# Performance work log

Hardware: AMD Instinct MI355X
Metric: run time of the kernel (lower is better)

The kernel has to match this reference:

```python
import jax, jax.numpy as jnp
import numpy as np

C = 16          # n_comp per axis
G = 300         # grid resolution per axis
N = 2_000_000   # number of sampled points


def setup_inputs() -> dict:
    key = jax.random.key(0)
    k1, k2, k3 = jax.random.split(key, 3)
    # normalized coordinates in [-1, 1] (grid_sample convention)
    xyz = jax.random.uniform(k1, (N, 3), minval=-1.0, maxval=1.0, dtype=jnp.float32)
    planes = 0.1 * jax.random.normal(k2, (3, C, G, G), dtype=jnp.float32)  # (axis, C, H, W)
    lines = 0.1 * jax.random.normal(k3, (3, C, G), dtype=jnp.float32)      # (axis, C, G)
    return {"xyz": xyz, "planes": planes, "lines": lines}


def _lerp_idx(coord, size):
    # align_corners=True mapping: [-1,1] -> [0, size-1]
    x = (coord + 1.0) * 0.5 * (size - 1)
    x0 = jnp.clip(jnp.floor(x), 0, size - 1).astype(jnp.int32)
    x1 = jnp.minimum(x0 + 1, size - 1)
    w = x - x0.astype(x.dtype)
    return x0, x1, w


def _sample_plane(plane, gx, gy):
    # plane: (C, H, W); gx, gy: (N,) in [-1,1]; grid x indexes W, y indexes H
    H, W = plane.shape[-2:]
    x0, x1, wx = _lerp_idx(gx, W)
    y0, y1, wy = _lerp_idx(gy, H)
    v00 = plane[:, y0, x0]  # (C, N)
    v01 = plane[:, y0, x1]
    v10 = plane[:, y1, x0]
    v11 = plane[:, y1, x1]
    return (v00 * (1 - wx) + v01 * wx) * (1 - wy) + (v10 * (1 - wx) + v11 * wx) * wy


def _sample_line(line, g):
    # line: (C, G); g: (N,) in [-1,1]; width dim of original (G,1) grid is size 1 -> ignored
    Gs = line.shape[-1]
    y0, y1, wy = _lerp_idx(g, Gs)
    return line[:, y0] * (1 - wy) + line[:, y1] * wy  # (C, N)


def reference(xyz, planes, lines):
    # matMode[i] = axes != i; plane i sampled at (x=xyz[id_0], y=xyz[id_1])
    matMode = ((1, 2), (0, 2), (0, 1))
    feats = []
    for i in range(3):
        a, b = matMode[i]
        p = _sample_plane(planes[i], xyz[:, a], xyz[:, b])  # (C, N)
        l = _sample_line(lines[i], xyz[:, i])               # (C, N)
        feats.append(p * l)
    return jnp.concatenate(feats, axis=0)  # (3*C, N)
```

## Files before the change

### kernel.cpp

```cpp
#include <hip/hip_runtime.h>

#define CC 16
#define GG 300

typedef unsigned int  u32;
typedef unsigned short u16;

__device__ __forceinline__ float bf_lo(u32 u) { union { u32 i; float f; } v; v.i = u << 16;          return v.f; }
__device__ __forceinline__ float bf_hi(u32 u) { union { u32 i; float f; } v; v.i = u & 0xffff0000u;  return v.f; }
__device__ __forceinline__ u16 f2bf(float f) {
    union { float f; u32 i; } v; v.f = f;
    u32 r = v.i + 0x7fffu + ((v.i >> 16) & 1u);
    return (u16)(r >> 16);
}

__global__ void transpose_planes_k(const float* __restrict__ src, u32* __restrict__ dst) {
    int tid = blockIdx.x * blockDim.x + threadIdx.x;
    const int total = 3 * GG * GG;
    if (tid >= total) return;
    int x = tid % GG;
    int y = (tid / GG) % GG;
    int i = tid / (GG * GG);
    u32 packed[8];
#pragma unroll
    for (int h = 0; h < 8; ++h) {
        float a = src[((size_t)(i * CC + 2 * h)     * GG + y) * GG + x];
        float b = src[((size_t)(i * CC + 2 * h + 1) * GG + y) * GG + x];
        packed[h] = (u32)f2bf(a) | ((u32)f2bf(b) << 16);
    }
    uint4* d = (uint4*)(dst + (size_t)tid * 8);
    d[0] = make_uint4(packed[0], packed[1], packed[2], packed[3]);
    d[1] = make_uint4(packed[4], packed[5], packed[6], packed[7]);
}

__global__ void transpose_lines_k(const float* __restrict__ src, u32* __restrict__ dst) {
    int tid = blockIdx.x * blockDim.x + threadIdx.x;
    const int total = 3 * GG;
    if (tid >= total) return;
    int g = tid % GG;
    int i = tid / GG;
    u32 packed[8];
#pragma unroll
    for (int h = 0; h < 8; ++h) {
        float a = src[(size_t)(i * CC + 2 * h)     * GG + g];
        float b = src[(size_t)(i * CC + 2 * h + 1) * GG + g];
        packed[h] = (u32)f2bf(a) | ((u32)f2bf(b) << 16);
    }
    uint4* d = (uint4*)(dst + (size_t)tid * 8);
    d[0] = make_uint4(packed[0], packed[1], packed[2], packed[3]);
    d[1] = make_uint4(packed[4], packed[5], packed[6], packed[7]);
}

__device__ __forceinline__ float bilerp(float v00, float v01, float v10, float v11,
                                        float wx, float wy) {
    float ox = 1.0f - wx, oy = 1.0f - wy;
    return (v00 * ox + v01 * wx) * oy + (v10 * ox + v11 * wx) * wy;
}

__global__ __launch_bounds__(256) void sample_k(
    const float* __restrict__ xyz,
    const u32* __restrict__ planesT,
    const u32* __restrict__ linesT,
    float* __restrict__ out, int N)
{
    int n = blockIdx.x * blockDim.x + threadIdx.x;
    if (n >= N) return;

    float crd[3];
    crd[0] = xyz[3 * n + 0];
    crd[1] = xyz[3 * n + 1];
    crd[2] = xyz[3 * n + 2];

    int i0[3], i1[3];
    float w[3];
#pragma unroll
    for (int k = 0; k < 3; ++k) {
        float xk = (crd[k] + 1.0f) * 0.5f * (float)(GG - 1);
        float xf = floorf(xk);
        xf = fminf(fmaxf(xf, 0.0f), (float)(GG - 1));
        i0[k] = (int)xf;
        i1[k] = min(i0[k] + 1, GG - 1);
        w[k] = xk - xf;
    }

    const int mata[3] = {1, 0, 0};
    const int matb[3] = {2, 2, 1};

#pragma unroll
    for (int i = 0; i < 3; ++i) {
        const int xa0 = i0[mata[i]], xa1 = i1[mata[i]];
        const int yb0 = i0[matb[i]], yb1 = i1[matb[i]];
        const float wx = w[mata[i]], wy = w[matb[i]], wz = w[i];
        const float oz = 1.0f - wz;

        const u32* pb = planesT + (size_t)i * (GG * GG * 8);
        const uint4* c00 = (const uint4*)(pb + (size_t)(yb0 * GG + xa0) * 8);
        const uint4* c01 = (const uint4*)(pb + (size_t)(yb0 * GG + xa1) * 8);
        const uint4* c10 = (const uint4*)(pb + (size_t)(yb1 * GG + xa0) * 8);
        const uint4* c11 = (const uint4*)(pb + (size_t)(yb1 * GG + xa1) * 8);
        const uint4* lp0 = (const uint4*)(linesT + ((size_t)i * GG + i0[i]) * 8);
        const uint4* lp1 = (const uint4*)(linesT + ((size_t)i * GG + i1[i]) * 8);

        uint4 A00 = c00[0], B00 = c00[1];
        uint4 A01 = c01[0], B01 = c01[1];
        uint4 A10 = c10[0], B10 = c10[1];
        uint4 A11 = c11[0], B11 = c11[1];
        uint4 AL0 = lp0[0], BL0 = lp0[1];
        uint4 AL1 = lp1[0], BL1 = lp1[1];

        u32 r00[8] = {A00.x, A00.y, A00.z, A00.w, B00.x, B00.y, B00.z, B00.w};
        u32 r01[8] = {A01.x, A01.y, A01.z, A01.w, B01.x, B01.y, B01.z, B01.w};
        u32 r10[8] = {A10.x, A10.y, A10.z, A10.w, B10.x, B10.y, B10.z, B10.w};
        u32 r11[8] = {A11.x, A11.y, A11.z, A11.w, B11.x, B11.y, B11.z, B11.w};
        u32 rl0[8] = {AL0.x, AL0.y, AL0.z, AL0.w, BL0.x, BL0.y, BL0.z, BL0.w};
        u32 rl1[8] = {AL1.x, AL1.y, AL1.z, AL1.w, BL1.x, BL1.y, BL1.z, BL1.w};

#pragma unroll
        for (int u = 0; u < 8; ++u) {
            float p0 = bilerp(bf_lo(r00[u]), bf_lo(r01[u]), bf_lo(r10[u]), bf_lo(r11[u]), wx, wy);
            float p1 = bilerp(bf_hi(r00[u]), bf_hi(r01[u]), bf_hi(r10[u]), bf_hi(r11[u]), wx, wy);
            float l0 = bf_lo(rl0[u]) * oz + bf_lo(rl1[u]) * wz;
            float l1 = bf_hi(rl0[u]) * oz + bf_hi(rl1[u]) * wz;
            size_t row = (size_t)(i * CC + 2 * u);
            __builtin_nontemporal_store(p0 * l0, &out[row * (size_t)N + n]);
            __builtin_nontemporal_store(p1 * l1, &out[(row + 1) * (size_t)N + n]);
        }
    }
}

__global__ __launch_bounds__(256) void sample_fallback_k(
    const float* __restrict__ xyz,
    const float* __restrict__ planes,
    const float* __restrict__ lines,
    float* __restrict__ out, int N)
{
    int n = blockIdx.x * blockDim.x + threadIdx.x;
    if (n >= N) return;

    float crd[3];
    crd[0] = xyz[3 * n + 0];
    crd[1] = xyz[3 * n + 1];
    crd[2] = xyz[3 * n + 2];

    int i0[3], i1[3];
    float w[3];
#pragma unroll
    for (int k = 0; k < 3; ++k) {
        float xk = (crd[k] + 1.0f) * 0.5f * (float)(GG - 1);
        float xf = floorf(xk);
        xf = fminf(fmaxf(xf, 0.0f), (float)(GG - 1));
        i0[k] = (int)xf;
        i1[k] = min(i0[k] + 1, GG - 1);
        w[k] = xk - xf;
    }

    const int mata[3] = {1, 0, 0};
    const int matb[3] = {2, 2, 1};

    for (int i = 0; i < 3; ++i) {
        const int xa0 = i0[mata[i]], xa1 = i1[mata[i]];
        const int yb0 = i0[matb[i]], yb1 = i1[matb[i]];
        const float wx = w[mata[i]], wy = w[matb[i]], wz = w[i];
        const float oz = 1.0f - wz;
        const float* pb = planes + (size_t)i * (CC * GG * GG);
        const float* lb = lines + (size_t)i * (CC * GG);
        for (int c = 0; c < CC; ++c) {
            const float* pc = pb + (size_t)c * (GG * GG);
            float p = bilerp(pc[yb0 * GG + xa0], pc[yb0 * GG + xa1],
                             pc[yb1 * GG + xa0], pc[yb1 * GG + xa1], wx, wy);
            float l = lb[c * GG + i0[i]] * oz + lb[c * GG + i1[i]] * wz;
            out[(size_t)(i * CC + c) * (size_t)N + n] = p * l;
        }
    }
}

extern "C" void kernel_launch(void* const* d_in, const int* in_sizes, int n_in,
                              void* d_out, int out_size, void* d_ws, size_t ws_size,
                              hipStream_t stream) {
    const float* xyz    = (const float*)d_in[0];
    const float* planes = (const float*)d_in[1];
    const float* lines  = (const float*)d_in[2];
    float* out = (float*)d_out;
    const int N = in_sizes[0] / 3;

    const size_t planesT_u32 = (size_t)3 * GG * GG * 8;
    const size_t linesT_u32  = (size_t)3 * GG * 8;
    const size_t need = (planesT_u32 + linesT_u32) * sizeof(u32);

    if (ws_size >= need) {
        u32* planesT = (u32*)d_ws;
        u32* linesT  = planesT + planesT_u32;
        {
            int total = 3 * GG * GG;
            transpose_planes_k<<<(total + 255) / 256, 256, 0, stream>>>(planes, planesT);
        }
        {
            int total = 3 * GG;
            transpose_lines_k<<<(total + 255) / 256, 256, 0, stream>>>(lines, linesT);
        }
        sample_k<<<(N + 255) / 256, 256, 0, stream>>>(xyz, planesT, linesT, out, N);
    } else {
        sample_fallback_k<<<(N + 255) / 256, 256, 0, stream>>>(xyz, planes, lines, out, N);
    }
}
```

Measured before the change: 623.0 us.

## Split sampling kernel across planes so each block handles one plane

The grid is now three times larger and each block processes a single plane for its 256 points, instead of one thread looping over all three planes. The aim is more parallelism and shorter per-thread dependency chains, with each block's gathers confined to one plane's transposed table so the cache works on a smaller footprint. The cost is that xyz is read and index/weight math is done three times per point. The xyz loads also become nontemporal, which may work against reuse of those coordinates across the three plane blocks.

```diff
diff --git a/kernel.cpp b/kernel.cpp
--- a/kernel.cpp
+++ b/kernel.cpp
@@ -57,19 +57,20 @@
     return (v00 * ox + v01 * wx) * oy + (v10 * ox + v11 * wx) * wy;
 }
 
-__global__ __launch_bounds__(256) void sample_k(
+__global__ __launch_bounds__(256) void sample_plane_k(
     const float* __restrict__ xyz,
     const u32* __restrict__ planesT,
     const u32* __restrict__ linesT,
-    float* __restrict__ out, int N)
+    float* __restrict__ out, int N, int nbPer)
 {
-    int n = blockIdx.x * blockDim.x + threadIdx.x;
+    const int plane = blockIdx.x / nbPer;
+    const int n = (blockIdx.x % nbPer) * 256 + threadIdx.x;
     if (n >= N) return;
 
     float crd[3];
-    crd[0] = xyz[3 * n + 0];
-    crd[1] = xyz[3 * n + 1];
-    crd[2] = xyz[3 * n + 2];
+    crd[0] = __builtin_nontemporal_load(xyz + 3 * (size_t)n + 0);
+    crd[1] = __builtin_nontemporal_load(xyz + 3 * (size_t)n + 1);
+    crd[2] = __builtin_nontemporal_load(xyz + 3 * (size_t)n + 2);
 
     int i0[3], i1[3];
     float w[3];
@@ -85,46 +86,45 @@
 
     const int mata[3] = {1, 0, 0};
     const int matb[3] = {2, 2, 1};
-
-#pragma unroll
-    for (int i = 0; i < 3; ++i) {
-        const int xa0 = i0[mata[i]], xa1 = i1[mata[i]];
-        const int yb0 = i0[matb[i]], yb1 = i1[matb[i]];
-        const float wx = w[mata[i]], wy = w[matb[i]], wz = w[i];
-        const float oz = 1.0f - wz;
-
-        const u32* pb = planesT + (size_t)i * (GG * GG * 8);
-        const uint4* c00 = (const uint4*)(pb + (size_t)(yb0 * GG + xa0) * 8);
-        const uint4* c01 = (const uint4*)(pb + (size_t)(yb0 * GG + xa1) * 8);
-        const uint4* c10 = (const uint4*)(pb + (size_t)(yb1 * GG + xa0) * 8);
-        const uint4* c11 = (const uint4*)(pb + (size_t)(yb1 * GG + xa1) * 8);
-        const uint4* lp0 = (const uint4*)(linesT + ((size_t)i * GG + i0[i]) * 8);
-        const uint4* lp1 = (const uint4*)(linesT + ((size_t)i * GG + i1[i]) * 8);
-
-        uint4 A00 = c00[0], B00 = c00[1];
-        uint4 A01 = c01[0], B01 = c01[1];
-        uint4 A10 = c10[0], B10 = c10[1];
-        uint4 A11 = c11[0], B11 = c11[1];
-        uint4 AL0 = lp0[0], BL0 = lp0[1];
-        uint4 AL1 = lp1[0], BL1 = lp1[1];
-
-        u32 r00[8] = {A00.x, A00.y, A00.z, A00.w, B00.x, B00.y, B00.z, B00.w};
-        u32 r01[8] = {A01.x, A01.y, A01.z, A01.w, B01.x, B01.y, B01.z, B01.w};
-        u32 r10[8] = {A10.x, A10.y, A10.z, A10.w, B10.x, B10.y, B10.z, B10.w};
-        u32 r11[8] = {A11.x, A11.y, A11.z, A11.w, B11.x, B11.y, B11.z, B11.w};
-        u32 rl0[8] = {AL0.x, AL0.y, AL0.z, AL0.w, BL0.x, BL0.y, BL0.z, BL0.w};
-        u32 rl1[8] = {AL1.x, AL1.y, AL1.z, AL1.w, BL1.x, BL1.y, BL1.z, BL1.w};
-
-#pragma unroll
-        for (int u = 0; u < 8; ++u) {
-            float p0 = bilerp(bf_lo(r00[u]), bf_lo(r01[u]), bf_lo(r10[u]), bf_lo(r11[u]), wx, wy);
-            float p1 = bilerp(bf_hi(r00[u]), bf_hi(r01[u]), bf_hi(r10[u]), bf_hi(r11[u]), wx, wy);
-            float l0 = bf_lo(rl0[u]) * oz + bf_lo(rl1[u]) * wz;
-            float l1 = bf_hi(rl0[u]) * oz + bf_hi(rl1[u]) * wz;
-            size_t row = (size_t)(i * CC + 2 * u);
-            __builtin_nontemporal_store(p0 * l0, &out[row * (size_t)N + n]);
-            __builtin_nontemporal_store(p1 * l1, &out[(row + 1) * (size_t)N + n]);
-        }
+    const int a = mata[plane];
+    const int b = matb[plane];
+
+    const int xa0 = i0[a], xa1 = i1[a];
+    const int yb0 = i0[b], yb1 = i1[b];
+    const float wx = w[a], wy = w[b], wz = w[plane];
+    const float oz = 1.0f - wz;
+
+    const u32* pb = planesT + (size_t)plane * (GG * GG * 8);
+    const uint4* c00 = (const uint4*)(pb + (size_t)(yb0 * GG + xa0) * 8);
+    const uint4* c01 = (const uint4*)(pb + (size_t)(yb0 * GG + xa1) * 8);
+    const uint4* c10 = (const uint4*)(pb + (size_t)(yb1 * GG + xa0) * 8);
+    const uint4* c11 = (const uint4*)(pb + (size_t)(yb1 * GG + xa1) * 8);
+    const uint4* lp0 = (const uint4*)(linesT + ((size_t)plane * GG + i0[plane]) * 8);
+    const uint4* lp1 = (const uint4*)(linesT + ((size_t)plane * GG + i1[plane]) * 8);
+
+    uint4 A00 = c00[0], B00 = c00[1];
+    uint4 A01 = c01[0], B01 = c01[1];
+    uint4 A10 = c10[0], B10 = c10[1];
+    uint4 A11 = c11[0], B11 = c11[1];
+    uint4 AL0 = lp0[0], BL0 = lp0[1];
+    uint4 AL1 = lp1[0], BL1 = lp1[1];
+
+    u32 r00[8] = {A00.x, A00.y, A00.z, A00.w, B00.x, B00.y, B00.z, B00.w};
+    u32 r01[8] = {A01.x, A01.y, A01.z, A01.w, B01.x, B01.y, B01.z, B01.w};
+    u32 r10[8] = {A10.x, A10.y, A10.z, A10.w, B10.x, B10.y, B10.z, B10.w};
+    u32 r11[8] = {A11.x, A11.y, A11.z, A11.w, B11.x, B11.y, B11.z, B11.w};
+    u32 rl0[8] = {AL0.x, AL0.y, AL0.z, AL0.w, BL0.x, BL0.y, BL0.z, BL0.w};
+    u32 rl1[8] = {AL1.x, AL1.y, AL1.z, AL1.w, BL1.x, BL1.y, BL1.z, BL1.w};
+
+#pragma unroll
+    for (int u = 0; u < 8; ++u) {
+        float p0 = bilerp(bf_lo(r00[u]), bf_lo(r01[u]), bf_lo(r10[u]), bf_lo(r11[u]), wx, wy);
+        float p1 = bilerp(bf_hi(r00[u]), bf_hi(r01[u]), bf_hi(r10[u]), bf_hi(r11[u]), wx, wy);
+        float l0 = bf_lo(rl0[u]) * oz + bf_lo(rl1[u]) * wz;
+        float l1 = bf_hi(rl0[u]) * oz + bf_hi(rl1[u]) * wz;
+        size_t row = (size_t)(plane * CC + 2 * u);
+        __builtin_nontemporal_store(p0 * l0, &out[row * (size_t)N + n]);
+        __builtin_nontemporal_store(p1 * l1, &out[(row + 1) * (size_t)N + n]);
     }
 }
 
@@ -198,7 +198,8 @@
             int total = 3 * GG;
             transpose_lines_k<<<(total + 255) / 256, 256, 0, stream>>>(lines, linesT);
         }
-        sample_k<<<(N + 255) / 256, 256, 0, stream>>>(xyz, planesT, linesT, out, N);
+        int nbPer = (N + 255) / 256;
+        sample_plane_k<<<3 * nbPer, 256, 0, stream>>>(xyz, planesT, linesT, out, N, nbPer);
     } else {
         sample_fallback_k<<<(N + 255) / 256, 256, 0, stream>>>(xyz, planes, lines, out, N);
     }
```

After: 542.9 us. 12.9% less time.
